# Kernel optimization log

Hardware: AMD Instinct MI355X
Metric: run time of the kernel (lower is better)

Reference implementation:

```python
import jax, jax.numpy as jnp
import numpy as np

N_NODES = 100000
N_EDGES = 1600000
NIN = 128
NHID = 128
N_GRAPHS = 1024


def _gcn_conv(x, src, dst, norm, W, b, n_nodes):
    """PyG-style GCNConv: linear (no bias) -> normalized scatter-add -> + bias."""
    xw = x @ W                                   # [N, out]
    msg = xw[src] * norm[:, None]                # gather + edge-normalize, [E', out]
    out = jax.ops.segment_sum(msg, dst, num_segments=n_nodes)
    return out + b


def _gcn_norm(edge_index, n_nodes):
    """Add self-loops and compute symmetric deg^{-1/2} normalization per edge."""
    loops = jnp.arange(n_nodes, dtype=edge_index.dtype)
    src = jnp.concatenate([edge_index[0], loops])
    dst = jnp.concatenate([edge_index[1], loops])
    deg = jax.ops.segment_sum(jnp.ones_like(dst, dtype=jnp.float32), dst,
                              num_segments=n_nodes)
    deg_isqrt = jnp.where(deg > 0, jax.lax.rsqrt(jnp.maximum(deg, 1.0)), 0.0)
    norm = deg_isqrt[src] * deg_isqrt[dst]
    return src, dst, norm


def setup_inputs() -> dict:
    key = jax.random.key(0)
    ks = jax.random.split(key, 8)
    x = jax.random.normal(ks[0], (N_NODES, NIN), dtype=jnp.float32)
    edge_index = jax.random.randint(ks[1], (2, N_EDGES), 0, N_NODES, dtype=jnp.int64)
    batch = jnp.sort(jax.random.randint(ks[2], (N_NODES,), 0, N_GRAPHS, dtype=jnp.int64))
    s_in = 1.0 / np.sqrt(NIN)
    s_h = 1.0 / np.sqrt(NHID)
    return {
        "x": x,
        "edge_index": edge_index,
        "batch": batch,
        "W1": jax.random.normal(ks[3], (NIN, NHID), dtype=jnp.float32) * s_in,
        "b1": jnp.zeros((NHID,), dtype=jnp.float32),
        "W2": jax.random.normal(ks[4], (NHID, NHID), dtype=jnp.float32) * s_h,
        "b2": jnp.zeros((NHID,), dtype=jnp.float32),
        "W3": jax.random.normal(ks[5], (NHID, NHID), dtype=jnp.float32) * s_h,
        "b3": jnp.zeros((NHID,), dtype=jnp.float32),
        "Wfc": jax.random.normal(ks[6], (NHID, 1), dtype=jnp.float32) * s_h,
        "bfc": jnp.zeros((1,), dtype=jnp.float32),
    }


def reference(x, edge_index, batch, W1, b1, W2, b2, W3, b3, Wfc, bfc):
    n_nodes = x.shape[0]
    src, dst, norm = _gcn_norm(edge_index, n_nodes)
    h = jax.nn.relu(_gcn_conv(x, src, dst, norm, W1, b1, n_nodes))
    h = jax.nn.relu(_gcn_conv(h, src, dst, norm, W2, b2, n_nodes))
    h = jax.nn.relu(_gcn_conv(h, src, dst, norm, W3, b3, n_nodes))
    # global mean pool over graphs in the batch
    sums = jax.ops.segment_sum(h, batch, num_segments=N_GRAPHS)      # [G, NHID]
    cnts = jax.ops.segment_sum(jnp.ones((n_nodes,), dtype=h.dtype), batch,
                               num_segments=N_GRAPHS)
    pooled = sums / jnp.maximum(cnts, 1.0)[:, None]
    return pooled @ Wfc + bfc                                        # [G, 1]
```

## Files before the change

### kernel.cpp

```cpp
#include <hip/hip_runtime.h>

#define N_NODES   100000
#define N_EDGES   1600000
#define NFEAT     128
#define N_GRAPHS  1024

#define BSHIFT  8
#define BNODES  256
#define NBUCK   391
#define BCAP    4608
#define SC_EDGES 4096
#define SC_EPT   8
#define SC_BLOCKS 391
#define BD_EPT   18

#define WT_STRIDE 136
#define GEMM_BLOCKS 782

typedef unsigned int uint32;
typedef unsigned short ushort;
typedef __attribute__((ext_vector_type(8))) short short8;
typedef __attribute__((ext_vector_type(4))) float f32x4;

__device__ inline ushort f2b(float f) {
    uint32 x = __float_as_uint(f);
    uint32 r = x + 0x7fffu + ((x >> 16) & 1u);
    return (ushort)(r >> 16);
}
__device__ inline float blo(uint32 u) { return __uint_as_float(u << 16); }
__device__ inline float bhi(uint32 u) { return __uint_as_float(u & 0xffff0000u); }

__device__ inline short8 cvt8(const float* p) {
    float4 v0 = ((const float4*)p)[0];
    float4 v1 = ((const float4*)p)[1];
    short8 r;
    r[0] = (short)f2b(v0.x); r[1] = (short)f2b(v0.y);
    r[2] = (short)f2b(v0.z); r[3] = (short)f2b(v0.w);
    r[4] = (short)f2b(v1.x); r[5] = (short)f2b(v1.y);
    r[6] = (short)f2b(v1.z); r[7] = (short)f2b(v1.w);
    return r;
}

__global__ __launch_bounds__(256) void k_castw(const float* __restrict__ W1, const float* __restrict__ W2,
                                               const float* __restrict__ W3, ushort* __restrict__ WT,
                                               int* __restrict__ cur) {
    int i = blockIdx.x * blockDim.x + threadIdx.x;
    if (i < NBUCK) cur[i] = 0;
    if (i >= 3 * NFEAT * NFEAT) return;
    int l = i >> 14;
    int j = i & 16383;
    int n = j >> 7;
    int k = j & 127;
    const float* W = (l == 0) ? W1 : (l == 1) ? W2 : W3;
    WT[i] = f2b(W[k * NFEAT + n]);
}

struct SMemScatter {
    int hist[NBUCK], gbase[NBUCK];
};

__global__ __launch_bounds__(512) void k_phase1(const int* __restrict__ src, const int* __restrict__ dst,
                                                int* __restrict__ cur, uint32* __restrict__ bbuf,
                                                const float* __restrict__ A, const ushort* __restrict__ WTl,
                                                ushort* __restrict__ C, int M) {
    __shared__ __align__(16) char smem[NFEAT * WT_STRIDE * 2];
    int t = threadIdx.x;
    if (blockIdx.x < SC_BLOCKS) {
        SMemScatter& S = *(SMemScatter*)smem;
        int e0 = blockIdx.x * SC_EDGES;
        int total = N_EDGES - e0; if (total > SC_EDGES) total = SC_EDGES; if (total < 0) total = 0;
        for (int i = t; i < NBUCK; i += 512) S.hist[i] = 0;
        __syncthreads();
        uint32 val[SC_EPT];
        int    meta[SC_EPT];
        #pragma unroll
        for (int k = 0; k < SC_EPT; ++k) {
            int i = t + k * 512;
            meta[k] = -1;
            if (i < total) {
                int s = src[e0 + i], d = dst[e0 + i];
                int b = d >> BSHIFT;
                int tk = atomicAdd(&S.hist[b], 1);
                val[k] = ((uint32)(d & (BNODES - 1)) << 17) | (uint32)s;
                meta[k] = (b << 13) | tk;
            }
        }
        __syncthreads();
        for (int i = t; i < NBUCK; i += 512) {
            int h = S.hist[i];
            if (h) S.gbase[i] = atomicAdd(&cur[i], h);
        }
        __syncthreads();
        #pragma unroll
        for (int k = 0; k < SC_EPT; ++k) {
            if (meta[k] >= 0) {
                int b = meta[k] >> 13;
                int addr = S.gbase[b] + (meta[k] & 0x1FFF);
                if (addr < BCAP)
                    bbuf[(size_t)b * BCAP + addr] = val[k];
            }
        }
    } else {
        ushort* sWT = (ushort*)smem;
        int gb = blockIdx.x - SC_BLOCKS;
        for (int i = t; i < NFEAT * 16; i += 512) {
            int n = i >> 4, c = i & 15;
            *(float4*)(sWT + n * WT_STRIDE + c * 8) = ((const float4*)WTl)[i];
        }
        int wave = t >> 6, lane = t & 63;
        int m0 = gb * 128 + wave * 16;
        int mRow = m0 + (lane & 15);
        if (mRow >= M) mRow = M - 1;
        int kg = lane >> 4;
        const float* Ap = A + (size_t)mRow * NFEAT + kg * 8;
        short8 a0 = cvt8(Ap);
        short8 a1 = cvt8(Ap + 32);
        short8 a2 = cvt8(Ap + 64);
        short8 a3 = cvt8(Ap + 96);
        __syncthreads();

        f32x4 acc[8];
        #pragma unroll
        for (int nt = 0; nt < 8; ++nt) acc[nt] = (f32x4){0.f, 0.f, 0.f, 0.f};
        #pragma unroll
        for (int nt = 0; nt < 8; ++nt) {
            int n = nt * 16 + (lane & 15);
            const short8* Bp = (const short8*)(sWT + n * WT_STRIDE + kg * 8);
            short8 b0 = Bp[0];
            short8 b1 = Bp[4];
            short8 b2 = Bp[8];
            short8 b3 = Bp[12];
            acc[nt] = __builtin_amdgcn_mfma_f32_16x16x32_bf16(a0, b0, acc[nt], 0, 0, 0);
            acc[nt] = __builtin_amdgcn_mfma_f32_16x16x32_bf16(a1, b1, acc[nt], 0, 0, 0);
            acc[nt] = __builtin_amdgcn_mfma_f32_16x16x32_bf16(a2, b2, acc[nt], 0, 0, 0);
            acc[nt] = __builtin_amdgcn_mfma_f32_16x16x32_bf16(a3, b3, acc[nt], 0, 0, 0);
        }
        __syncthreads();
        {
            int colBase = lane & 15;
            #pragma unroll
            for (int r = 0; r < 4; ++r) {
                int lr = wave * 16 + kg * 4 + r;
                #pragma unroll
                for (int nt = 0; nt < 8; ++nt)
                    sWT[lr * NFEAT + nt * 16 + colBase] = f2b(acc[nt][r]);
            }
        }
        __syncthreads();
        {
            int rowBase = gb * 128;
            const float4* sC4 = (const float4*)sWT;
            for (int i = t; i < 2048; i += 512) {
                int row = i >> 4;
                int gr = rowBase + row;
                if (gr < M) ((float4*)(C + (size_t)gr * NFEAT))[i & 15] = sC4[i];
            }
        }
    }
}

__global__ __launch_bounds__(256) void k_build(const uint32* __restrict__ bbuf, const int* __restrict__ cur,
                                               int* __restrict__ col, int* __restrict__ offsets,
                                               float* __restrict__ dinv) {
    int b = blockIdx.x;
    __shared__ int hist[BNODES], excl[BNODES];
    __shared__ int wsum[4], wtot[4];
    __shared__ int sBase, sTotal;
    int t = threadIdx.x;
    {
        int pre = 0, tot = 0;
        #pragma unroll
        for (int q = 0; q < 2; ++q) {
            int i = 2 * t + q;
            if (i < NBUCK) {
                int v = cur[i]; if (v > BCAP) v = BCAP;
                tot += v;
                if (i < b) pre += v;
            }
        }
        int lane = t & 63, w = t >> 6;
        #pragma unroll
        for (int d = 32; d > 0; d >>= 1) { pre += __shfl_down(pre, d, 64); tot += __shfl_down(tot, d, 64); }
        if (lane == 0) { wsum[w] = pre; wtot[w] = tot; }
        __syncthreads();
        if (t == 0) {
            sBase = wsum[0] + wsum[1] + wsum[2] + wsum[3];
            sTotal = wtot[0] + wtot[1] + wtot[2] + wtot[3];
        }
        hist[t] = 0;
    }
    __syncthreads();
    int base = sBase;
    if (b == NBUCK - 1 && t == 0) offsets[N_NODES] = sTotal;
    int cnt = cur[b]; if (cnt > BCAP) cnt = BCAP;
    const uint32* reg = bbuf + (size_t)b * BCAP;

    uint32 val[BD_EPT];
    int    meta[BD_EPT];
    #pragma unroll
    for (int k = 0; k < BD_EPT; ++k) {
        int i = t + k * 256;
        meta[k] = -1;
        if (i < cnt) {
            uint32 p = reg[i];
            int node = p >> 17;
            int tk = atomicAdd(&hist[node], 1);
            val[k] = p & 0x1FFFF;
            meta[k] = (node << 16) | tk;
        }
    }
    __syncthreads();
    {
        int c = hist[t];
        int lane = t & 63, w = t >> 6;
        int inc = c;
        #pragma unroll
        for (int d = 1; d < 64; d <<= 1) {
            int u = __shfl_up(inc, d, 64);
            if (lane >= d) inc += u;
        }
        if (lane == 63) wsum[w] = inc;
        __syncthreads();
        int wpre = 0;
        for (int i = 0; i < w; ++i) wpre += wsum[i];
        int e = wpre + inc - c;
        excl[t] = e;
        int node = (b << BSHIFT) + t;
        if (node < N_NODES) {
            offsets[node] = base + e;
            dinv[node] = rsqrtf((float)(c + 1));
        }
    }
    __syncthreads();
    #pragma unroll
    for (int k = 0; k < BD_EPT; ++k) {
        if (meta[k] >= 0) {
            int node = meta[k] >> 16;
            col[base + excl[node] + (meta[k] & 0xFFFF)] = (int)val[k];
        }
    }
}

#define AGG_GROUP4 \
    int half = lane >> 4; \
    int fl = lane & 15; \
    float dn = dinv[n]; \
    int e0 = off[n], e1 = off[n + 1]; \
    int deg = e1 - e0; \
    int maxd = deg; \
    { int u16 = __shfl_xor(maxd, 16, 64); if (u16 > maxd) maxd = u16; \
      int u32 = __shfl_xor(maxd, 32, 64); if (u32 > maxd) maxd = u32; } \
    const uint4* XW4 = (const uint4*)XWu; \
    uint4 sv = XW4[(size_t)n * 16 + fl]; \
    float ws = dn * dn; \
    float a0 = ws * blo(sv.x), a1 = ws * bhi(sv.x); \
    float a2 = ws * blo(sv.y), a3 = ws * bhi(sv.y); \
    float a4 = ws * blo(sv.z), a5 = ws * bhi(sv.z); \
    float a6 = ws * blo(sv.w), a7 = ws * bhi(sv.w); \
    int cm = 0; float wm = 0.f; \
    if (fl < deg) { cm = col[e0 + fl]; wm = dn * dinv[cm]; } \
    for (int base = 0; base < maxd; base += 16) { \
        int nb = base + 16; \
        int cmn = 0; float wmn = 0.f; \
        if (nb + fl < deg) { cmn = col[e0 + nb + fl]; wmn = dn * dinv[cmn]; } \
        int lim = maxd - base; if (lim > 16) lim = 16; \
        for (int j = 0; j < lim; j += 8) { \
            uint4 u[8]; float w[8]; \
            _Pragma("unroll") \
            for (int p = 0; p < 8; ++p) { \
                int sl = (half << 4) + j + p; \
                int cc = __shfl(cm, sl, 64); \
                w[p] = __shfl(wm, sl, 64); \
                u[p] = XW4[(size_t)cc * 16 + fl]; \
            } \
            _Pragma("unroll") \
            for (int p = 0; p < 8; ++p) { \
                a0 = fmaf(w[p], blo(u[p].x), a0); a1 = fmaf(w[p], bhi(u[p].x), a1); \
                a2 = fmaf(w[p], blo(u[p].y), a2); a3 = fmaf(w[p], bhi(u[p].y), a3); \
                a4 = fmaf(w[p], blo(u[p].z), a4); a5 = fmaf(w[p], bhi(u[p].z), a5); \
                a6 = fmaf(w[p], blo(u[p].w), a6); a7 = fmaf(w[p], bhi(u[p].w), a7); \
            } \
        } \
        cm = cmn; wm = wmn; \
    }

__global__ __launch_bounds__(256) void k_agg_gemm(const uint32* __restrict__ XWu,
                                                  const int* __restrict__ col,
                                                  const int* __restrict__ off,
                                                  const float* __restrict__ dinv,
                                                  const float* __restrict__ bias,
                                                  const ushort* __restrict__ WTl,
                                                  ushort* __restrict__ C) {
    __shared__ __align__(16) ushort sA[16 * WT_STRIDE];
    int t = threadIdx.x;
    int lane = t & 63;
    int lw = t >> 6;
    int n = (blockIdx.x << 4) + (lw << 2) + (lane >> 4);
    AGG_GROUP4
    {
        float4 bb0 = ((const float4*)bias)[2 * fl];
        float4 bb1 = ((const float4*)bias)[2 * fl + 1];
        float r0 = fmaxf(a0 + bb0.x, 0.f), r1 = fmaxf(a1 + bb0.y, 0.f);
        float r2 = fmaxf(a2 + bb0.z, 0.f), r3 = fmaxf(a3 + bb0.w, 0.f);
        float r4 = fmaxf(a4 + bb1.x, 0.f), r5 = fmaxf(a5 + bb1.y, 0.f);
        float r6 = fmaxf(a6 + bb1.z, 0.f), r7 = fmaxf(a7 + bb1.w, 0.f);
        uint4 o;
        o.x = (uint32)f2b(r0) | ((uint32)f2b(r1) << 16);
        o.y = (uint32)f2b(r2) | ((uint32)f2b(r3) << 16);
        o.z = (uint32)f2b(r4) | ((uint32)f2b(r5) << 16);
        o.w = (uint32)f2b(r6) | ((uint32)f2b(r7) << 16);
        int lrow = (lw << 2) + half;
        *(uint4*)(sA + lrow * WT_STRIDE + fl * 8) = o;
    }
    __syncthreads();
    {
        const short8* Ap = (const short8*)(sA + fl * WT_STRIDE + half * 8);
        short8 af0 = Ap[0];
        short8 af1 = Ap[4];
        short8 af2 = Ap[8];
        short8 af3 = Ap[12];
        f32x4 acc[2];
        acc[0] = (f32x4){0.f, 0.f, 0.f, 0.f};
        acc[1] = (f32x4){0.f, 0.f, 0.f, 0.f};
        #pragma unroll
        for (int q = 0; q < 2; ++q) {
            int nt = lw * 2 + q;
            const short8* Bp = (const short8*)(WTl + (nt * 16 + fl) * NFEAT + half * 8);
            short8 b0 = Bp[0];
            short8 b1 = Bp[4];
            short8 b2 = Bp[8];
            short8 b3 = Bp[12];
            acc[q] = __builtin_amdgcn_mfma_f32_16x16x32_bf16(af0, b0, acc[q], 0, 0, 0);
            acc[q] = __builtin_amdgcn_mfma_f32_16x16x32_bf16(af1, b1, acc[q], 0, 0, 0);
            acc[q] = __builtin_amdgcn_mfma_f32_16x16x32_bf16(af2, b2, acc[q], 0, 0, 0);
            acc[q] = __builtin_amdgcn_mfma_f32_16x16x32_bf16(af3, b3, acc[q], 0, 0, 0);
        }
        __syncthreads();
        #pragma unroll
        for (int q = 0; q < 2; ++q) {
            int nt = lw * 2 + q;
            #pragma unroll
            for (int r = 0; r < 4; ++r)
                sA[(half * 4 + r) * NFEAT + nt * 16 + fl] = f2b(acc[q][r]);
        }
    }
    __syncthreads();
    {
        int row = t >> 4;
        float4 v = ((const float4*)sA)[t];
        ((float4*)(C + (size_t)((blockIdx.x << 4) + row) * NFEAT))[t & 15] = v;
    }
}

__global__ __launch_bounds__(256) void k_agg_fc(const uint32* __restrict__ XWu, const int* __restrict__ col,
                                                const int* __restrict__ off, const float* __restrict__ dinv,
                                                const float* __restrict__ bias, const float* __restrict__ Wfc,
                                                float* __restrict__ nodeS) {
    int wid = (blockIdx.x * blockDim.x + threadIdx.x) >> 6;
    int lane = threadIdx.x & 63;
    int n = (wid << 2) + (lane >> 4);
    if (n >= N_NODES) return;
    AGG_GROUP4
    float4 bb0 = ((const float4*)bias)[2 * fl];
    float4 bb1 = ((const float4*)bias)[2 * fl + 1];
    float4 wf0 = ((const float4*)Wfc)[2 * fl];
    float4 wf1 = ((const float4*)Wfc)[2 * fl + 1];
    float s = fmaxf(a0 + bb0.x, 0.f) * wf0.x + fmaxf(a1 + bb0.y, 0.f) * wf0.y
            + fmaxf(a2 + bb0.z, 0.f) * wf0.z + fmaxf(a3 + bb0.w, 0.f) * wf0.w
            + fmaxf(a4 + bb1.x, 0.f) * wf1.x + fmaxf(a5 + bb1.y, 0.f) * wf1.y
            + fmaxf(a6 + bb1.z, 0.f) * wf1.z + fmaxf(a7 + bb1.w, 0.f) * wf1.w;
    s += __shfl_xor(s, 8, 64);
    s += __shfl_xor(s, 4, 64);
    s += __shfl_xor(s, 2, 64);
    s += __shfl_xor(s, 1, 64);
    if (fl == 0) nodeS[n] = s;
}

__device__ inline int lower_bound_dev(const int* a, int n, int key) {
    int lo = 0, hi = n;
    while (lo < hi) {
        int mid = (lo + hi) >> 1;
        if (a[mid] < key) lo = mid + 1; else hi = mid;
    }
    return lo;
}

__global__ __launch_bounds__(256) void k_pool(const float* __restrict__ nodeS, const int* __restrict__ batch,
                                              const float* __restrict__ bfc, float* __restrict__ out) {
    int g = blockIdx.x;
    int t = threadIdx.x;
    int lo = lower_bound_dev(batch, N_NODES, g);
    int hi = lower_bound_dev(batch, N_NODES, g + 1);
    float s = 0.f;
    for (int i = lo + t; i < hi; i += 256) s += nodeS[i];
    for (int d = 32; d > 0; d >>= 1) s += __shfl_down(s, d, 64);
    __shared__ float ws[4];
    int lane = t & 63, w = t >> 6;
    if (lane == 0) ws[w] = s;
    __syncthreads();
    if (t == 0) {
        float tot = ws[0] + ws[1] + ws[2] + ws[3];
        float cnt = (float)(hi - lo);
        out[g] = tot / fmaxf(cnt, 1.0f) + bfc[0];
    }
}

extern "C" void kernel_launch(void* const* d_in, const int* in_sizes, int n_in,
                              void* d_out, int out_size, void* d_ws, size_t ws_size,
                              hipStream_t stream) {
    const float* x    = (const float*)d_in[0];
    const int*   ei   = (const int*)d_in[1];
    const int*   batch= (const int*)d_in[2];
    const float* W1   = (const float*)d_in[3];
    const float* b1   = (const float*)d_in[4];
    const float* W2   = (const float*)d_in[5];
    const float* b2   = (const float*)d_in[6];
    const float* W3   = (const float*)d_in[7];
    const float* b3   = (const float*)d_in[8];
    const float* Wfc  = (const float*)d_in[9];
    const float* bfc  = (const float*)d_in[10];
    float* out = (float*)d_out;

    const int* src = ei;
    const int* dst = ei + N_EDGES;

    char* p = (char*)d_ws;
    auto carve = [&](size_t bytes) { void* r = (void*)p; p += (bytes + 255) & ~(size_t)255; return r; };
    int*    cur       = (int*)   carve(sizeof(int) * NBUCK);
    uint32* bbuf      = (uint32*)carve(sizeof(uint32) * (size_t)NBUCK * BCAP);
    float*  dinv      = (float*) carve(sizeof(float) * N_NODES);
    int*    offsets   = (int*)   carve(sizeof(int) * (N_NODES + 1));
    int*    col       = (int*)   carve(sizeof(int) * N_EDGES);
    ushort* XW        = (ushort*)carve(sizeof(short) * (size_t)N_NODES * NFEAT);
    ushort* XW2       = (ushort*)carve(sizeof(short) * (size_t)N_NODES * NFEAT);
    ushort* WT        = (ushort*)carve(sizeof(short) * 3 * NFEAT * NFEAT);
    float*  nodeS     = (float*) carve(sizeof(float) * N_NODES);

    const int aggBlocks = N_NODES / 16;

    k_castw<<<(3 * NFEAT * NFEAT + 255) / 256, 256, 0, stream>>>(W1, W2, W3, WT, cur);
    k_phase1<<<SC_BLOCKS + GEMM_BLOCKS, 512, 0, stream>>>(src, dst, cur, bbuf, x, WT, XW, N_NODES);
    k_build<<<NBUCK, 256, 0, stream>>>(bbuf, cur, col, offsets, dinv);

    k_agg_gemm<<<aggBlocks, 256, 0, stream>>>((const uint32*)XW, col, offsets, dinv, b1,
                                              WT + NFEAT * NFEAT, XW2);
    k_agg_gemm<<<aggBlocks, 256, 0, stream>>>((const uint32*)XW2, col, offsets, dinv, b2,
                                              WT + 2 * NFEAT * NFEAT, XW);
    k_agg_fc<<<aggBlocks, 256, 0, stream>>>((const uint32*)XW, col, offsets, dinv, b3, Wfc, nodeS);

    k_pool<<<N_GRAPHS, 256, 0, stream>>>(nodeS, batch, bfc, out);
}
```

Measured before the change: 354.1 us.

## Fold weight cast, pool, and count setup into existing kernels; atomic pooling

```diff
diff --git a/kernel.cpp b/kernel.cpp
--- a/kernel.cpp
+++ b/kernel.cpp
@@ -41,31 +41,29 @@
     return r;
 }
 
-__global__ __launch_bounds__(256) void k_castw(const float* __restrict__ W1, const float* __restrict__ W2,
-                                               const float* __restrict__ W3, ushort* __restrict__ WT,
-                                               int* __restrict__ cur) {
-    int i = blockIdx.x * blockDim.x + threadIdx.x;
-    if (i < NBUCK) cur[i] = 0;
-    if (i >= 3 * NFEAT * NFEAT) return;
-    int l = i >> 14;
-    int j = i & 16383;
-    int n = j >> 7;
-    int k = j & 127;
-    const float* W = (l == 0) ? W1 : (l == 1) ? W2 : W3;
-    WT[i] = f2b(W[k * NFEAT + n]);
-}
-
 struct SMemScatter {
     int hist[NBUCK], gbase[NBUCK];
 };
 
 __global__ __launch_bounds__(512) void k_phase1(const int* __restrict__ src, const int* __restrict__ dst,
                                                 int* __restrict__ cur, uint32* __restrict__ bbuf,
-                                                const float* __restrict__ A, const ushort* __restrict__ WTl,
+                                                const float* __restrict__ A,
+                                                const float* __restrict__ W1, const float* __restrict__ W2,
+                                                const float* __restrict__ W3, ushort* __restrict__ WT,
                                                 ushort* __restrict__ C, int M) {
     __shared__ __align__(16) char smem[NFEAT * WT_STRIDE * 2];
     int t = threadIdx.x;
     if (blockIdx.x < SC_BLOCKS) {
+        {
+            int ci = blockIdx.x * 512 + t;
+            if (ci < 2 * NFEAT * NFEAT) {
+                int l = 1 + (ci >> 14);
+                int j = ci & 16383;
+                int n = j >> 7, k = j & 127;
+                const float* W = (l == 1) ? W2 : W3;
+                WT[(l << 14) + j] = f2b(W[k * NFEAT + n]);
+            }
+        }
         SMemScatter& S = *(SMemScatter*)smem;
         int e0 = blockIdx.x * SC_EDGES;
         int total = N_EDGES - e0; if (total > SC_EDGES) total = SC_EDGES; if (total < 0) total = 0;
@@ -103,9 +101,9 @@
     } else {
         ushort* sWT = (ushort*)smem;
         int gb = blockIdx.x - SC_BLOCKS;
-        for (int i = t; i < NFEAT * 16; i += 512) {
-            int n = i >> 4, c = i & 15;
-            *(float4*)(sWT + n * WT_STRIDE + c * 8) = ((const float4*)WTl)[i];
+        for (int i = t; i < NFEAT * NFEAT; i += 512) {
+            int k = i >> 7, n = i & 127;
+            sWT[n * WT_STRIDE + k] = f2b(W1[k * NFEAT + n]);
         }
         int wave = t >> 6, lane = t & 63;
         int m0 = gb * 128 + wave * 16;
@@ -159,14 +157,35 @@
     }
 }
 
+__device__ inline int lower_bound_dev(const int* a, int n, int key) {
+    int lo = 0, hi = n;
+    while (lo < hi) {
+        int mid = (lo + hi) >> 1;
+        if (a[mid] < key) lo = mid + 1; else hi = mid;
+    }
+    return lo;
+}
+
 __global__ __launch_bounds__(256) void k_build(const uint32* __restrict__ bbuf, const int* __restrict__ cur,
                                                int* __restrict__ col, int* __restrict__ offsets,
-                                               float* __restrict__ dinv) {
+                                               float* __restrict__ dinv,
+                                               const int* __restrict__ batch, const float* __restrict__ bfc,
+                                               float* __restrict__ out, float* __restrict__ cinv) {
     int b = blockIdx.x;
+    int t = threadIdx.x;
+    if (b >= NBUCK) {
+        int g = ((b - NBUCK) << 8) + t;
+        if (g < N_GRAPHS) {
+            int lo = lower_bound_dev(batch, N_NODES, g);
+            int hi = lower_bound_dev(batch, N_NODES, g + 1);
+            cinv[g] = 1.0f / fmaxf((float)(hi - lo), 1.0f);
+            out[g] = bfc[0];
+        }
+        return;
+    }
     __shared__ int hist[BNODES], excl[BNODES];
     __shared__ int wsum[4], wtot[4];
     __shared__ int sBase, sTotal;
-    int t = threadIdx.x;
     {
         int pre = 0, tot = 0;
         #pragma unroll
@@ -355,7 +374,8 @@
 __global__ __launch_bounds__(256) void k_agg_fc(const uint32* __restrict__ XWu, const int* __restrict__ col,
                                                 const int* __restrict__ off, const float* __restrict__ dinv,
                                                 const float* __restrict__ bias, const float* __restrict__ Wfc,
-                                                float* __restrict__ nodeS) {
+                                                const int* __restrict__ batch, const float* __restrict__ cinv,
+                                                float* __restrict__ out) {
     int wid = (blockIdx.x * blockDim.x + threadIdx.x) >> 6;
     int lane = threadIdx.x & 63;
     int n = (wid << 2) + (lane >> 4);
@@ -373,35 +393,9 @@
     s += __shfl_xor(s, 4, 64);
     s += __shfl_xor(s, 2, 64);
     s += __shfl_xor(s, 1, 64);
-    if (fl == 0) nodeS[n] = s;
-}
-
-__device__ inline int lower_bound_dev(const int* a, int n, int key) {
-    int lo = 0, hi = n;
-    while (lo < hi) {
-        int mid = (lo + hi) >> 1;
-        if (a[mid] < key) lo = mid + 1; else hi = mid;
-    }
-    return lo;
-}
-
-__global__ __launch_bounds__(256) void k_pool(const float* __restrict__ nodeS, const int* __restrict__ batch,
-                                              const float* __restrict__ bfc, float* __restrict__ out) {
-    int g = blockIdx.x;
-    int t = threadIdx.x;
-    int lo = lower_bound_dev(batch, N_NODES, g);
-    int hi = lower_bound_dev(batch, N_NODES, g + 1);
-    float s = 0.f;
-    for (int i = lo + t; i < hi; i += 256) s += nodeS[i];
-    for (int d = 32; d > 0; d >>= 1) s += __shfl_down(s, d, 64);
-    __shared__ float ws[4];
-    int lane = t & 63, w = t >> 6;
-    if (lane == 0) ws[w] = s;
-    __syncthreads();
-    if (t == 0) {
-        float tot = ws[0] + ws[1] + ws[2] + ws[3];
-        float cnt = (float)(hi - lo);
-        out[g] = tot / fmaxf(cnt, 1.0f) + bfc[0];
+    if (fl == 0) {
+        int g = batch[n];
+        atomicAdd(&out[g], s * cinv[g]);
     }
 }
 
@@ -434,19 +428,19 @@
     ushort* XW        = (ushort*)carve(sizeof(short) * (size_t)N_NODES * NFEAT);
     ushort* XW2       = (ushort*)carve(sizeof(short) * (size_t)N_NODES * NFEAT);
     ushort* WT        = (ushort*)carve(sizeof(short) * 3 * NFEAT * NFEAT);
-    float*  nodeS     = (float*) carve(sizeof(float) * N_NODES);
+    float*  cinv      = (float*) carve(sizeof(float) * N_GRAPHS);
 
     const int aggBlocks = N_NODES / 16;
 
-    k_castw<<<(3 * NFEAT * NFEAT + 255) / 256, 256, 0, stream>>>(W1, W2, W3, WT, cur);
-    k_phase1<<<SC_BLOCKS + GEMM_BLOCKS, 512, 0, stream>>>(src, dst, cur, bbuf, x, WT, XW, N_NODES);
-    k_build<<<NBUCK, 256, 0, stream>>>(bbuf, cur, col, offsets, dinv);
+    hipMemsetAsync(cur, 0, sizeof(int) * NBUCK, stream);
+    k_phase1<<<SC_BLOCKS + GEMM_BLOCKS, 512, 0, stream>>>(src, dst, cur, bbuf, x, W1, W2, W3,
+                                                          WT, XW, N_NODES);
+    k_build<<<NBUCK + 4, 256, 0, stream>>>(bbuf, cur, col, offsets, dinv, batch, bfc, out, cinv);
 
     k_agg_gemm<<<aggBlocks, 256, 0, stream>>>((const uint32*)XW, col, offsets, dinv, b1,
                                               WT + NFEAT * NFEAT, XW2);
     k_agg_gemm<<<aggBlocks, 256, 0, stream>>>((const uint32*)XW2, col, offsets, dinv, b2,
                                               WT + 2 * NFEAT * NFEAT, XW);
-    k_agg_fc<<<aggBlocks, 256, 0, stream>>>((const uint32*)XW, col, offsets, dinv, b3, Wfc, nodeS);
-
-    k_pool<<<N_GRAPHS, 256, 0, stream>>>(nodeS, batch, bfc, out);
-}
+    k_agg_fc<<<aggBlocks, 256, 0, stream>>>((const uint32*)XW, col, offsets, dinv, b3, Wfc,
+                                            batch, cinv, out);
+}
```

Measured after the change: 422.3 us. +19.3%, slower.

## Split fused scatter/GEMM kernel and fold weight casts into producers

Applied to the files above, without the earlier changes.

```diff
diff --git a/kernel.cpp b/kernel.cpp
--- a/kernel.cpp
+++ b/kernel.cpp
@@ -41,120 +41,117 @@
     return r;
 }
 
-__global__ __launch_bounds__(256) void k_castw(const float* __restrict__ W1, const float* __restrict__ W2,
-                                               const float* __restrict__ W3, ushort* __restrict__ WT,
-                                               int* __restrict__ cur) {
-    int i = blockIdx.x * blockDim.x + threadIdx.x;
-    if (i < NBUCK) cur[i] = 0;
-    if (i >= 3 * NFEAT * NFEAT) return;
-    int l = i >> 14;
-    int j = i & 16383;
-    int n = j >> 7;
-    int k = j & 127;
-    const float* W = (l == 0) ? W1 : (l == 1) ? W2 : W3;
-    WT[i] = f2b(W[k * NFEAT + n]);
-}
-
 struct SMemScatter {
     int hist[NBUCK], gbase[NBUCK];
 };
 
-__global__ __launch_bounds__(512) void k_phase1(const int* __restrict__ src, const int* __restrict__ dst,
-                                                int* __restrict__ cur, uint32* __restrict__ bbuf,
-                                                const float* __restrict__ A, const ushort* __restrict__ WTl,
-                                                ushort* __restrict__ C, int M) {
-    __shared__ __align__(16) char smem[NFEAT * WT_STRIDE * 2];
+__global__ __launch_bounds__(512) void k_scatter_cast(const int* __restrict__ src, const int* __restrict__ dst,
+                                                      int* __restrict__ cur, uint32* __restrict__ bbuf,
+                                                      const float* __restrict__ W2, const float* __restrict__ W3,
+                                                      ushort* __restrict__ WT) {
+    __shared__ SMemScatter S;
     int t = threadIdx.x;
-    if (blockIdx.x < SC_BLOCKS) {
-        SMemScatter& S = *(SMemScatter*)smem;
-        int e0 = blockIdx.x * SC_EDGES;
-        int total = N_EDGES - e0; if (total > SC_EDGES) total = SC_EDGES; if (total < 0) total = 0;
-        for (int i = t; i < NBUCK; i += 512) S.hist[i] = 0;
-        __syncthreads();
-        uint32 val[SC_EPT];
-        int    meta[SC_EPT];
-        #pragma unroll
-        for (int k = 0; k < SC_EPT; ++k) {
-            int i = t + k * 512;
-            meta[k] = -1;
-            if (i < total) {
-                int s = src[e0 + i], d = dst[e0 + i];
-                int b = d >> BSHIFT;
-                int tk = atomicAdd(&S.hist[b], 1);
-                val[k] = ((uint32)(d & (BNODES - 1)) << 17) | (uint32)s;
-                meta[k] = (b << 13) | tk;
-            }
-        }
-        __syncthreads();
-        for (int i = t; i < NBUCK; i += 512) {
-            int h = S.hist[i];
-            if (h) S.gbase[i] = atomicAdd(&cur[i], h);
-        }
-        __syncthreads();
-        #pragma unroll
-        for (int k = 0; k < SC_EPT; ++k) {
-            if (meta[k] >= 0) {
-                int b = meta[k] >> 13;
-                int addr = S.gbase[b] + (meta[k] & 0x1FFF);
-                if (addr < BCAP)
-                    bbuf[(size_t)b * BCAP + addr] = val[k];
-            }
-        }
-    } else {
-        ushort* sWT = (ushort*)smem;
-        int gb = blockIdx.x - SC_BLOCKS;
-        for (int i = t; i < NFEAT * 16; i += 512) {
-            int n = i >> 4, c = i & 15;
-            *(float4*)(sWT + n * WT_STRIDE + c * 8) = ((const float4*)WTl)[i];
-        }
-        int wave = t >> 6, lane = t & 63;
-        int m0 = gb * 128 + wave * 16;
-        int mRow = m0 + (lane & 15);
-        if (mRow >= M) mRow = M - 1;
-        int kg = lane >> 4;
-        const float* Ap = A + (size_t)mRow * NFEAT + kg * 8;
-        short8 a0 = cvt8(Ap);
-        short8 a1 = cvt8(Ap + 32);
-        short8 a2 = cvt8(Ap + 64);
-        short8 a3 = cvt8(Ap + 96);
-        __syncthreads();
-
-        f32x4 acc[8];
-        #pragma unroll
-        for (int nt = 0; nt < 8; ++nt) acc[nt] = (f32x4){0.f, 0.f, 0.f, 0.f};
-        #pragma unroll
-        for (int nt = 0; nt < 8; ++nt) {
-            int n = nt * 16 + (lane & 15);
-            const short8* Bp = (const short8*)(sWT + n * WT_STRIDE + kg * 8);
-            short8 b0 = Bp[0];
-            short8 b1 = Bp[4];
-            short8 b2 = Bp[8];
-            short8 b3 = Bp[12];
-            acc[nt] = __builtin_amdgcn_mfma_f32_16x16x32_bf16(a0, b0, acc[nt], 0, 0, 0);
-            acc[nt] = __builtin_amdgcn_mfma_f32_16x16x32_bf16(a1, b1, acc[nt], 0, 0, 0);
-            acc[nt] = __builtin_amdgcn_mfma_f32_16x16x32_bf16(a2, b2, acc[nt], 0, 0, 0);
-            acc[nt] = __builtin_amdgcn_mfma_f32_16x16x32_bf16(a3, b3, acc[nt], 0, 0, 0);
-        }
-        __syncthreads();
-        {
-            int colBase = lane & 15;
+    {
+        int ci = blockIdx.x * 512 + t;
+        if (ci < 2 * NFEAT * NFEAT) {
+            int l = 1 + (ci >> 14);
+            int j = ci & 16383;
+            int n = j >> 7, k = j & 127;
+            const float* W = (l == 1) ? W2 : W3;
+            WT[(l << 14) + j] = f2b(W[k * NFEAT + n]);
+        }
+    }
+    int e0 = blockIdx.x * SC_EDGES;
+    int total = N_EDGES - e0; if (total > SC_EDGES) total = SC_EDGES; if (total < 0) total = 0;
+    for (int i = t; i < NBUCK; i += 512) S.hist[i] = 0;
+    __syncthreads();
+    uint32 val[SC_EPT];
+    int    meta[SC_EPT];
+    #pragma unroll
+    for (int k = 0; k < SC_EPT; ++k) {
+        int i = t + k * 512;
+        meta[k] = -1;
+        if (i < total) {
+            int s = src[e0 + i], d = dst[e0 + i];
+            int b = d >> BSHIFT;
+            int tk = atomicAdd(&S.hist[b], 1);
+            val[k] = ((uint32)(d & (BNODES - 1)) << 17) | (uint32)s;
+            meta[k] = (b << 13) | tk;
+        }
+    }
+    __syncthreads();
+    for (int i = t; i < NBUCK; i += 512) {
+        int h = S.hist[i];
+        if (h) S.gbase[i] = atomicAdd(&cur[i], h);
+    }
+    __syncthreads();
+    #pragma unroll
+    for (int k = 0; k < SC_EPT; ++k) {
+        if (meta[k] >= 0) {
+            int b = meta[k] >> 13;
+            int addr = S.gbase[b] + (meta[k] & 0x1FFF);
+            if (addr < BCAP)
+                bbuf[(size_t)b * BCAP + addr] = val[k];
+        }
+    }
+}
+
+__global__ __launch_bounds__(512) void k_gemm1(const float* __restrict__ A, const float* __restrict__ W1,
+                                               ushort* __restrict__ C, int M) {
+    __shared__ __align__(16) ushort sWT[NFEAT * WT_STRIDE];
+    int t = threadIdx.x;
+    int gb = blockIdx.x;
+    for (int i = t; i < NFEAT * NFEAT; i += 512) {
+        int k = i >> 7, n = i & 127;
+        sWT[n * WT_STRIDE + k] = f2b(W1[k * NFEAT + n]);
+    }
+    int wave = t >> 6, lane = t & 63;
+    int m0 = gb * 128 + wave * 16;
+    int mRow = m0 + (lane & 15);
+    if (mRow >= M) mRow = M - 1;
+    int kg = lane >> 4;
+    const float* Ap = A + (size_t)mRow * NFEAT + kg * 8;
+    short8 a0 = cvt8(Ap);
+    short8 a1 = cvt8(Ap + 32);
+    short8 a2 = cvt8(Ap + 64);
+    short8 a3 = cvt8(Ap + 96);
+    __syncthreads();
+
+    f32x4 acc[8];
+    #pragma unroll
+    for (int nt = 0; nt < 8; ++nt) acc[nt] = (f32x4){0.f, 0.f, 0.f, 0.f};
+    #pragma unroll
+    for (int nt = 0; nt < 8; ++nt) {
+        int n = nt * 16 + (lane & 15);
+        const short8* Bp = (const short8*)(sWT + n * WT_STRIDE + kg * 8);
+        short8 b0 = Bp[0];
+        short8 b1 = Bp[4];
+        short8 b2 = Bp[8];
+        short8 b3 = Bp[12];
+        acc[nt] = __builtin_amdgcn_mfma_f32_16x16x32_bf16(a0, b0, acc[nt], 0, 0, 0);
+        acc[nt] = __builtin_amdgcn_mfma_f32_16x16x32_bf16(a1, b1, acc[nt], 0, 0, 0);
+        acc[nt] = __builtin_amdgcn_mfma_f32_16x16x32_bf16(a2, b2, acc[nt], 0, 0, 0);
+        acc[nt] = __builtin_amdgcn_mfma_f32_16x16x32_bf16(a3, b3, acc[nt], 0, 0, 0);
+    }
+    __syncthreads();
+    {
+        int colBase = lane & 15;
+        #pragma unroll
+        for (int r = 0; r < 4; ++r) {
+            int lr = wave * 16 + kg * 4 + r;
             #pragma unroll
-            for (int r = 0; r < 4; ++r) {
-                int lr = wave * 16 + kg * 4 + r;
-                #pragma unroll
-                for (int nt = 0; nt < 8; ++nt)
-                    sWT[lr * NFEAT + nt * 16 + colBase] = f2b(acc[nt][r]);
-            }
-        }
-        __syncthreads();
-        {
-            int rowBase = gb * 128;
-            const float4* sC4 = (const float4*)sWT;
-            for (int i = t; i < 2048; i += 512) {
-                int row = i >> 4;
-                int gr = rowBase + row;
-                if (gr < M) ((float4*)(C + (size_t)gr * NFEAT))[i & 15] = sC4[i];
-            }
+            for (int nt = 0; nt < 8; ++nt)
+                sWT[lr * NFEAT + nt * 16 + colBase] = f2b(acc[nt][r]);
+        }
+    }
+    __syncthreads();
+    {
+        int rowBase = gb * 128;
+        const float4* sC4 = (const float4*)sWT;
+        for (int i = t; i < 2048; i += 512) {
+            int row = i >> 4;
+            int gr = rowBase + row;
+            if (gr < M) ((float4*)(C + (size_t)gr * NFEAT))[i & 15] = sC4[i];
         }
     }
 }
@@ -438,8 +435,9 @@
 
     const int aggBlocks = N_NODES / 16;
 
-    k_castw<<<(3 * NFEAT * NFEAT + 255) / 256, 256, 0, stream>>>(W1, W2, W3, WT, cur);
-    k_phase1<<<SC_BLOCKS + GEMM_BLOCKS, 512, 0, stream>>>(src, dst, cur, bbuf, x, WT, XW, N_NODES);
+    hipMemsetAsync(cur, 0, sizeof(int) * NBUCK, stream);
+    k_scatter_cast<<<SC_BLOCKS, 512, 0, stream>>>(src, dst, cur, bbuf, W2, W3, WT);
+    k_gemm1<<<GEMM_BLOCKS, 512, 0, stream>>>(x, W1, XW, N_NODES);
     k_build<<<NBUCK, 256, 0, stream>>>(bbuf, cur, col, offsets, dinv);
 
     k_agg_gemm<<<aggBlocks, 256, 0, stream>>>((const uint32*)XW, col, offsets, dinv, b1,
```

After: 365.5 us. 3.2% more time.
